# Optimization experiments

Hardware: AMD Instinct MI355X
Metric: run time of the kernel (lower is better)

## Reference

```python
import jax, jax.numpy as jnp
import numpy as np

EMBED_DIM = 1024
NUM_HEADS = 16
HEAD_DIM = EMBED_DIM // NUM_HEADS
SCALING = HEAD_DIM ** -0.5


def setup_inputs() -> dict:
    key = jax.random.key(0)
    ks = jax.random.split(key, 10)
    B, S, D = 2, 2048, EMBED_DIM
    lim = 1.0 / np.sqrt(D)  # torch Linear default init scale
    def lin(k):
        kw, kb = jax.random.split(k)
        W = jax.random.uniform(kw, (D, D), jnp.float32, -lim, lim)
        b = jax.random.uniform(kb, (D,), jnp.float32, -lim, lim)
        return W, b
    Wq, bq = lin(ks[0])
    Wk, bk = lin(ks[1])
    Wv, bv = lin(ks[2])
    Wo, bo = lin(ks[3])
    hidden_states = jax.random.normal(ks[4], (B, S, D), jnp.float32)
    attention_mask = jnp.ones((B, S), jnp.int32)  # unused by the module's forward
    return {"hidden_states": hidden_states, "attention_mask": attention_mask,
            "Wq": Wq, "bq": bq, "Wk": Wk, "bk": bk, "Wv": Wv, "bv": bv,
            "Wo": Wo, "bo": bo}


def reference(hidden_states, attention_mask, Wq, bq, Wk, bk, Wv, bv, Wo, bo):
    B, S, D = hidden_states.shape
    H, hd = NUM_HEADS, HEAD_DIM

    def split_heads(x):  # [B,S,D] -> [B,H,S,hd]
        return x.reshape(B, S, H, hd).transpose(0, 2, 1, 3)

    q = split_heads(hidden_states @ Wq.T + bq) * SCALING
    k = split_heads(hidden_states @ Wk.T + bk)
    v = split_heads(hidden_states @ Wv.T + bv)

    scores = jnp.einsum("bhqd,bhkd->bhqk", q, k)  # [B,H,S,S]
    mask_value = jnp.finfo(scores.dtype).min
    causal = jnp.triu(jnp.ones((S, S), bool), k=1)  # True above diagonal
    scores = jnp.where(causal, mask_value, scores)
    probs = jax.nn.softmax(scores, axis=-1)

    out = jnp.einsum("bhqk,bhkd->bhqd", probs, v)  # [B,H,S,hd]
    out = out.transpose(0, 2, 1, 3).reshape(B, S, D)
    return out @ Wo.T + bo
```

## Files before the change

### kernel.cpp

```cpp
#include <hip/hip_runtime.h>


typedef __bf16 bf16;
typedef __attribute__((ext_vector_type(8))) __bf16 bf16x8;
typedef __attribute__((ext_vector_type(4))) __bf16 bf16x4;
typedef __attribute__((ext_vector_type(4))) float f32x4;

#define MFMA16(a, b, c) __builtin_amdgcn_mfma_f32_16x16x32_bf16((a), (b), (c), 0, 0, 0)

__device__ __forceinline__ void gl_lds16(const bf16* g, bf16* l) {
  __builtin_amdgcn_global_load_lds(
      (__attribute__((address_space(1))) void*)g,
      (__attribute__((address_space(3))) void*)l, 16, 0, 0);
}

__global__ __launch_bounds__(256) void cvt5(
    const float* __restrict__ x, const float* __restrict__ wq,
    const float* __restrict__ wk, const float* __restrict__ wv,
    const float* __restrict__ wo,
    bf16* __restrict__ xb, bf16* __restrict__ wqb, bf16* __restrict__ wkb,
    bf16* __restrict__ wvb, bf16* __restrict__ wob) {
  const int bx = blockIdx.x;
  const float* s;
  bf16* d;
  int base;
  if (bx < 4096)      { s = x;  d = xb;  base = bx; }
  else if (bx < 5120) { s = wq; d = wqb; base = bx - 4096; }
  else if (bx < 6144) { s = wk; d = wkb; base = bx - 5120; }
  else if (bx < 7168) { s = wv; d = wvb; base = bx - 6144; }
  else                { s = wo; d = wob; base = bx - 7168; }
  const int i = base * 1024 + threadIdx.x * 4;
  const float4 v = *(const float4*)(s + i);
  bf16x4 o;
  o[0] = (bf16)v.x; o[1] = (bf16)v.y; o[2] = (bf16)v.z; o[3] = (bf16)v.w;
  *(bf16x4*)(d + i) = o;
}

__global__ __launch_bounds__(256) void vtrans(const bf16* __restrict__ v,
                                              bf16* __restrict__ vt) {
  __shared__ bf16 Ts[64 * 80];
  const int t = threadIdx.x;
  const int st = blockIdx.x;
  const int bh = blockIdx.y;
  const int bb = bh >> 4, h = bh & 15;
  const bf16* src = v + ((size_t)bb * 2048 + st * 64) * 1024 + h * 64;
#pragma unroll
  for (int i = 0; i < 2; ++i) {
    const int idx = i * 256 + t;
    const int sl = idx >> 3, c = idx & 7;
    *(bf16x8*)&Ts[sl * 80 + c * 8] = *(const bf16x8*)(src + (size_t)sl * 1024 + c * 8);
  }
  __syncthreads();
  bf16* dst = vt + (size_t)bh * 64 * 2048 + st * 64;
#pragma unroll
  for (int i = 0; i < 2; ++i) {
    const int idx = i * 256 + t;
    const int d = idx >> 3, c2 = idx & 7;
    bf16x8 tmp;
#pragma unroll
    for (int e = 0; e < 8; ++e) tmp[e] = Ts[(c2 * 8 + e) * 80 + d];
    *(bf16x8*)(dst + (size_t)d * 2048 + c2 * 8) = tmp;
  }
}

template <int BM, typename OutT>
__global__ __launch_bounds__(256, 2) void gemm_bt3(
    const bf16* __restrict__ A,
    const bf16* __restrict__ W0, const bf16* __restrict__ W1, const bf16* __restrict__ W2,
    const float* __restrict__ B0, const float* __restrict__ B1, const float* __restrict__ B2,
    OutT* __restrict__ O0, OutT* __restrict__ O1, OutT* __restrict__ O2,
    float s0, float s1, float s2, int K) {
  constexpr int WM = BM / 32;
  __shared__ bf16 As[BM * 32];
  __shared__ bf16 Bs[128 * 32];

  const int t = threadIdx.x;
  const int lane = t & 63;
  const int wv = t >> 6;
  const int wm = wv & 1, wn = wv >> 1;
  const int qd = lane >> 4, ln = lane & 15;

  const int which = blockIdx.x >> 3;
  const bf16* W = (which == 0) ? W0 : (which == 1) ? W1 : W2;
  const float* Bi = (which == 0) ? B0 : (which == 1) ? B1 : B2;
  OutT* O = (which == 0) ? O0 : (which == 1) ? O1 : O2;
  const float scale = (which == 0) ? s0 : (which == 1) ? s1 : s2;

  const int n0 = (blockIdx.x & 7) * 128;
  const int m0 = blockIdx.y * BM;

  f32x4 acc[WM][4] = {};

  const bf16* ga = A + (size_t)(m0 + (t >> 2)) * K + (t & 3) * 8;
  const bf16* gb = W + (size_t)(n0 + (t >> 2)) * K + (t & 3) * 8;
  bf16* lA = &As[t * 8];
  bf16* lB = &Bs[t * 8];

  for (int k0 = 0; k0 < K; k0 += 32) {
#pragma unroll
    for (int i = 0; i < BM / 64; ++i)
      gl_lds16(ga + (size_t)i * 64 * K + k0, lA + i * 2048);
#pragma unroll
    for (int i = 0; i < 2; ++i)
      gl_lds16(gb + (size_t)i * 64 * K + k0, lB + i * 2048);
    __syncthreads();

    bf16x8 af[WM], bw[4];
#pragma unroll
    for (int i = 0; i < WM; ++i)
      af[i] = *(const bf16x8*)&As[(wm * (BM / 2) + i * 16 + ln) * 32 + qd * 8];
#pragma unroll
    for (int j = 0; j < 4; ++j)
      bw[j] = *(const bf16x8*)&Bs[(wn * 64 + j * 16 + ln) * 32 + qd * 8];
#pragma unroll
    for (int i = 0; i < WM; ++i)
#pragma unroll
      for (int j = 0; j < 4; ++j)
        acc[i][j] = MFMA16(af[i], bw[j], acc[i][j]);
    __syncthreads();
  }

#pragma unroll
  for (int i = 0; i < WM; ++i) {
    const int row = m0 + wm * (BM / 2) + i * 16 + qd * 4;
#pragma unroll
    for (int j = 0; j < 4; ++j) {
      const int col = n0 + wn * 64 + j * 16 + ln;
      const float bias = Bi[col];
#pragma unroll
      for (int r = 0; r < 4; ++r) {
        const float v = (acc[i][j][r] + bias) * scale;
        O[(size_t)(row + r) * 1024 + col] = (OutT)v;
      }
    }
  }
}

__global__ __launch_bounds__(256, 4) void attn_causal(
    const bf16* __restrict__ Q, const bf16* __restrict__ Kg,
    const bf16* __restrict__ VT, bf16* __restrict__ Ob) {
  __shared__ bf16 Ks[2][64 * 64];
  __shared__ bf16 Vts[2][64 * 64];
  __shared__ bf16 Ps[4][16 * 64];

  const int t = threadIdx.x;
  const int lane = t & 63;
  const int w = t >> 6;
  const int qd = lane >> 4, ln = lane & 15;

  const int blk = blockIdx.x;
  const int bh = blk & 31;
  const int tq = 31 - (blk >> 5);
  const int bb = bh >> 4, h = bh & 15;
  const size_t rowbase = (size_t)bb * 2048;
  const bf16* vtb = VT + (size_t)bh * 64 * 2048;

  const int q0 = tq * 64;
  const int nj = tq + 1;

  auto stage = [&](int buf, int j) {
    const bf16* kp = Kg + (rowbase + j * 64) * 1024 + h * 64;
#pragma unroll
    for (int i = 0; i < 2; ++i) {
      const int s = i * 256 + t;
      const int kv = s >> 3;
      const int c = (s & 7) ^ (kv & 7);
      gl_lds16(kp + (size_t)kv * 1024 + c * 8, &Ks[buf][s * 8]);
    }
#pragma unroll
    for (int i = 0; i < 2; ++i) {
      const int s = i * 256 + t;
      const int d = s >> 3;
      const int c = (s & 7) ^ (d & 7);
      gl_lds16(vtb + (size_t)d * 2048 + j * 64 + c * 8, &Vts[buf][s * 8]);
    }
  };

  const bf16* qp = Q + (rowbase + q0 + w * 16) * 1024 + h * 64;
  bf16x8 qf[2];
#pragma unroll
  for (int ks = 0; ks < 2; ++ks)
    qf[ks] = *(const bf16x8*)(qp + (size_t)ln * 1024 + ks * 32 + qd * 8);

  float l_run[4] = {0.f, 0.f, 0.f, 0.f};
  f32x4 accO[4] = {};

  stage(0, 0);

#pragma unroll 1
  for (int j = 0; j < nj; ++j) {
    const int buf = j & 1;
    __syncthreads();
    if (j + 1 < nj) stage(buf ^ 1, j + 1);

    f32x4 accS[4] = {};
#pragma unroll
    for (int ks = 0; ks < 2; ++ks) {
#pragma unroll
      for (int nt = 0; nt < 4; ++nt) {
        const bf16x8 bk = *(const bf16x8*)
            &Ks[buf][(nt * 16 + ln) * 64 + (((ks * 4 + qd) ^ (ln & 7)) << 3)];
        accS[nt] = MFMA16(qf[ks], bk, accS[nt]);
      }
    }

    const bool dom = (j == nj - 1);
#pragma unroll
    for (int r = 0; r < 4; ++r) {
      const int row = qd * 4 + r;
      const int qg = q0 + w * 16 + row;
      float sum = 0.f;
#pragma unroll
      for (int nt = 0; nt < 4; ++nt) {
        float p = __expf(accS[nt][r]);
        const int col = nt * 16 + ln;
        if (dom && (j * 64 + col) > qg) p = 0.f;
        sum += p;
        Ps[w][row * 64 + ((((col >> 3) ^ (row & 7))) << 3) + (col & 7)] = (bf16)p;
      }
      l_run[r] += sum;
    }

#pragma unroll
    for (int kt = 0; kt < 2; ++kt) {
      const bf16x8 ap = *(const bf16x8*)
          &Ps[w][ln * 64 + (((kt * 4 + qd) ^ (ln & 7)) << 3)];
#pragma unroll
      for (int nt = 0; nt < 4; ++nt) {
        const bf16x8 bv = *(const bf16x8*)
            &Vts[buf][(nt * 16 + ln) * 64 + (((kt * 4 + qd) ^ (ln & 7)) << 3)];
        accO[nt] = MFMA16(ap, bv, accO[nt]);
      }
    }
  }

  bf16* op = Ob + (rowbase + q0 + w * 16) * 1024 + h * 64;
#pragma unroll
  for (int r = 0; r < 4; ++r) {
    float l = l_run[r];
#pragma unroll
    for (int off = 1; off < 16; off <<= 1) l += __shfl_xor(l, off, 64);
    const float inv_l = 1.0f / l;
#pragma unroll
    for (int nt = 0; nt < 4; ++nt)
      op[(size_t)(qd * 4 + r) * 1024 + nt * 16 + ln] = (bf16)(accO[nt][r] * inv_l);
  }
}

extern "C" void kernel_launch(void* const* d_in, const int* in_sizes, int n_in,
                              void* d_out, int out_size, void* d_ws, size_t ws_size,
                              hipStream_t stream) {
  const float* X  = (const float*)d_in[0];
  const float* Wq = (const float*)d_in[2];
  const float* bq = (const float*)d_in[3];
  const float* Wk = (const float*)d_in[4];
  const float* bk = (const float*)d_in[5];
  const float* Wv = (const float*)d_in[6];
  const float* bv = (const float*)d_in[7];
  const float* Wo = (const float*)d_in[8];
  const float* bo = (const float*)d_in[9];
  float* out = (float*)d_out;

  bf16* xb  = (bf16*)d_ws;
  bf16* wqb = xb  + (size_t)4096 * 1024;
  bf16* wkb = wqb + (size_t)1024 * 1024;
  bf16* wvb = wkb + (size_t)1024 * 1024;
  bf16* wob = wvb + (size_t)1024 * 1024;
  bf16* q   = wob + (size_t)1024 * 1024;
  bf16* k   = q   + (size_t)4096 * 1024;
  bf16* v   = k   + (size_t)4096 * 1024;
  bf16* vt  = v   + (size_t)4096 * 1024;
  bf16* ao  = xb;

  const float scaling = 0.125f;

  dim3 blk(256);
  cvt5<<<dim3(8192), blk, 0, stream>>>(X, Wq, Wk, Wv, Wo, xb, wqb, wkb, wvb, wob);
  gemm_bt3<128, bf16><<<dim3(24, 32), blk, 0, stream>>>(
      xb, wqb, wkb, wvb, bq, bk, bv, q, k, v, scaling, 1.f, 1.f, 1024);
  vtrans<<<dim3(32, 32), blk, 0, stream>>>(v, vt);
  attn_causal<<<dim3(1024), blk, 0, stream>>>(q, k, vt, ao);
  gemm_bt3<64, float><<<dim3(8, 64), blk, 0, stream>>>(
      ao, wob, wob, wob, bo, bo, bo, out, out, out, 1.f, 1.f, 1.f, 1024);
}
```

Before: 191.4 us.

## Widen GEMM K-tile with swizzled LDS, reorder attention tiles, split mask path

The projection GEMM now stages a K-slice of 64 instead of 32 per iteration. LDS rows are XOR-swizzled to avoid bank conflicts, and there are two MFMA k-steps per barrier pair, which halves the synchronisation count but doubles shared memory per block. The causal attention kernel changes the block-to-query-tile order into a zigzag pattern, meant to balance long and short causal rows across concurrently resident blocks. The softmax exponent loop is also split into a masked diagonal branch and an unmasked branch, removing per-element mask checks on off-diagonal tiles.

```diff
diff --git a/kernel.cpp b/kernel.cpp
--- a/kernel.cpp
+++ b/kernel.cpp
@@ -71,8 +71,8 @@
     OutT* __restrict__ O0, OutT* __restrict__ O1, OutT* __restrict__ O2,
     float s0, float s1, float s2, int K) {
   constexpr int WM = BM / 32;
-  __shared__ bf16 As[BM * 32];
-  __shared__ bf16 Bs[128 * 32];
+  __shared__ bf16 As[BM * 64];
+  __shared__ bf16 Bs[128 * 64];
 
   const int t = threadIdx.x;
   const int lane = t & 63;
@@ -91,32 +91,42 @@
 
   f32x4 acc[WM][4] = {};
 
-  const bf16* ga = A + (size_t)(m0 + (t >> 2)) * K + (t & 3) * 8;
-  const bf16* gb = W + (size_t)(n0 + (t >> 2)) * K + (t & 3) * 8;
-  bf16* lA = &As[t * 8];
-  bf16* lB = &Bs[t * 8];
-
-  for (int k0 = 0; k0 < K; k0 += 32) {
-#pragma unroll
-    for (int i = 0; i < BM / 64; ++i)
-      gl_lds16(ga + (size_t)i * 64 * K + k0, lA + i * 2048);
-#pragma unroll
-    for (int i = 0; i < 2; ++i)
-      gl_lds16(gb + (size_t)i * 64 * K + k0, lB + i * 2048);
+  for (int k0 = 0; k0 < K; k0 += 64) {
+#pragma unroll
+    for (int i = 0; i < BM / 32; ++i) {
+      const int s = i * 256 + t;
+      const int row = s >> 3;
+      const int c = (s & 7) ^ (row & 7);
+      gl_lds16(A + (size_t)(m0 + row) * K + k0 + c * 8, &As[s * 8]);
+    }
+#pragma unroll
+    for (int i = 0; i < 4; ++i) {
+      const int s = i * 256 + t;
+      const int row = s >> 3;
+      const int c = (s & 7) ^ (row & 7);
+      gl_lds16(W + (size_t)(n0 + row) * K + k0 + c * 8, &Bs[s * 8]);
+    }
     __syncthreads();
 
-    bf16x8 af[WM], bw[4];
-#pragma unroll
-    for (int i = 0; i < WM; ++i)
-      af[i] = *(const bf16x8*)&As[(wm * (BM / 2) + i * 16 + ln) * 32 + qd * 8];
-#pragma unroll
-    for (int j = 0; j < 4; ++j)
-      bw[j] = *(const bf16x8*)&Bs[(wn * 64 + j * 16 + ln) * 32 + qd * 8];
-#pragma unroll
-    for (int i = 0; i < WM; ++i)
-#pragma unroll
-      for (int j = 0; j < 4; ++j)
-        acc[i][j] = MFMA16(af[i], bw[j], acc[i][j]);
+#pragma unroll
+    for (int ks = 0; ks < 2; ++ks) {
+      bf16x8 af[WM], bw[4];
+#pragma unroll
+      for (int i = 0; i < WM; ++i) {
+        const int r = wm * (BM / 2) + i * 16 + ln;
+        af[i] = *(const bf16x8*)&As[r * 64 + (((ks * 4 + qd) ^ (ln & 7)) << 3)];
+      }
+#pragma unroll
+      for (int j = 0; j < 4; ++j) {
+        const int r = wn * 64 + j * 16 + ln;
+        bw[j] = *(const bf16x8*)&Bs[r * 64 + (((ks * 4 + qd) ^ (ln & 7)) << 3)];
+      }
+#pragma unroll
+      for (int i = 0; i < WM; ++i)
+#pragma unroll
+        for (int j = 0; j < 4; ++j)
+          acc[i][j] = MFMA16(af[i], bw[j], acc[i][j]);
+    }
     __syncthreads();
   }
 
@@ -150,7 +160,9 @@
 
   const int blk = blockIdx.x;
   const int bh = blk & 31;
-  const int tq = 31 - (blk >> 5);
+  const int g = blk >> 5;
+  const int a = g & 7, b = g >> 3;
+  const int tq = (b == 0) ? (31 - a) : (b == 1) ? (16 + a) : (b == 2) ? (15 - a) : a;
   const int bb = bh >> 4, h = bh & 15;
   const size_t rowbase = (size_t)bb * 2048;
   const bf16* vtb = VT + (size_t)bh * 64 * 2048;
@@ -204,21 +216,36 @@
       }
     }
 
-    const bool dom = (j == nj - 1);
-#pragma unroll
-    for (int r = 0; r < 4; ++r) {
-      const int row = qd * 4 + r;
-      const int qg = q0 + w * 16 + row;
-      float sum = 0.f;
-#pragma unroll
-      for (int nt = 0; nt < 4; ++nt) {
-        float p = __expf(accS[nt][r]);
-        const int col = nt * 16 + ln;
-        if (dom && (j * 64 + col) > qg) p = 0.f;
-        sum += p;
-        Ps[w][row * 64 + ((((col >> 3) ^ (row & 7))) << 3) + (col & 7)] = (bf16)p;
-      }
-      l_run[r] += sum;
+    if (j == nj - 1) {
+#pragma unroll
+      for (int r = 0; r < 4; ++r) {
+        const int row = qd * 4 + r;
+        const int qg = q0 + w * 16 + row;
+        float sum = 0.f;
+#pragma unroll
+        for (int nt = 0; nt < 4; ++nt) {
+          float p = __expf(accS[nt][r]);
+          const int col = nt * 16 + ln;
+          if ((j * 64 + col) > qg) p = 0.f;
+          sum += p;
+          Ps[w][row * 64 + ((((col >> 3) ^ (row & 7))) << 3) + (col & 7)] = (bf16)p;
+        }
+        l_run[r] += sum;
+      }
+    } else {
+#pragma unroll
+      for (int r = 0; r < 4; ++r) {
+        const int row = qd * 4 + r;
+        float sum = 0.f;
+#pragma unroll
+        for (int nt = 0; nt < 4; ++nt) {
+          const float p = __expf(accS[nt][r]);
+          const int col = nt * 16 + ln;
+          sum += p;
+          Ps[w][row * 64 + ((((col >> 3) ^ (row & 7))) << 3) + (col & 7)] = (bf16)p;
+        }
+        l_run[r] += sum;
+      }
     }
 
 #pragma unroll
```

New measurement: 190.4 us. About the same (-0.5%).
